# Optimization experiments

Measured on AMD Instinct MI355X. Metric: run time of the kernel, lower is better.

Reference implementation:

```python
import jax, jax.numpy as jnp
import numpy as np

# ---- constants mirroring the module config ----
TIMESTEPS = 1000
N_GT = 3            # GT phases {stable, pre-shock, shock}
NUM_EXPERTS = 6     # 2 sub-experts per GT phase; phase L -> experts {L, L+3}
LAMBDA_REG = 0.01
LAMBDA_LB = 0.01
PHASE_WEIGHTS = np.array([1.0, 5.0, 5.0], dtype=np.float32)


def _sinusoidal_embed(t, dim):
    # standard DDPM sinusoidal timestep embedding -> [B, dim]
    half = dim // 2
    freqs = jnp.exp(-jnp.log(10000.0) * jnp.arange(half, dtype=jnp.float32) / half)
    args = t.astype(jnp.float32)[:, None] * freqs[None, :]
    return jnp.concatenate([jnp.sin(args), jnp.cos(args)], axis=-1)


def _alphas_bar():
    betas = jnp.linspace(1e-4, 0.02, TIMESTEPS, dtype=jnp.float32)
    return jnp.cumprod(1.0 - betas)


def setup_inputs() -> dict:
    B, Tp, Tf, Df, Ds, dm, E, H = 512, 256, 64, 64, 32, 512, NUM_EXPERTS, 512
    key = jax.random.key(0)
    ks = jax.random.split(key, 16)
    s = 0.02  # init scale
    d_in = Df + 2 * dm  # noisy features + global ctx + t embedding
    return {
        'observed_data': jax.random.normal(ks[0], (B, Tp, Df), jnp.float32),
        'future_data':   jax.random.normal(ks[1], (B, Tf, Df), jnp.float32),
        'static_context': jax.random.normal(ks[2], (B, Ds), jnp.float32),
        'eps':           jax.random.normal(ks[3], (B, Tf, Df), jnp.float32),
        'phase_label':   jax.random.randint(ks[4], (B,), 0, N_GT),
        't':             jax.random.randint(ks[5], (B,), 0, TIMESTEPS),
        'W_enc':    jax.random.normal(ks[6], (Df, dm), jnp.float32) * s,
        'b_enc':    jnp.zeros((dm,), jnp.float32),
        'W_stat':   jax.random.normal(ks[7], (Ds, dm), jnp.float32) * s,
        'W_router': jax.random.normal(ks[8], (dm, E), jnp.float32) * s,
        'b_router': jnp.zeros((E,), jnp.float32),
        'W1': jax.random.normal(ks[9],  (E, d_in, H), jnp.float32) * s,
        'b1': jnp.zeros((E, H), jnp.float32),
        'W2': jax.random.normal(ks[10], (E, H, Df), jnp.float32) * s,
        'b2': jnp.zeros((E, Df), jnp.float32),
    }


def reference(observed_data, future_data, static_context, eps,
              W_enc, b_enc, W_stat, W_router, b_router,
              W1, b1, W2, b2, phase_label, t):
    B, Tf, Df = future_data.shape
    E = W1.shape[0]
    dm = W_enc.shape[1]

    # ---- frozen encoder (torch.no_grad in the original) ----
    ctx_seq = jax.nn.gelu(observed_data @ W_enc + (static_context @ W_stat)[:, None, :] + b_enc)  # [B,Tp,dm]
    global_ctx = ctx_seq.mean(axis=1)                                                             # [B,dm]
    ctx_seq = jax.lax.stop_gradient(ctx_seq)
    global_ctx = jax.lax.stop_gradient(global_ctx)

    # ---- router (trainable) ----
    router_logits = global_ctx @ W_router + b_router        # [B,E]
    router_probs = jax.nn.softmax(router_logits, axis=-1)

    # ---- GT-masked top-1 routing: phase p -> argmax over experts {p, p+3} ----
    selected = jnp.zeros((B,), jnp.int32)
    for p in range(N_GT):
        sub = jnp.stack([router_probs[:, p], router_probs[:, p + N_GT]], axis=1)  # [B,2]
        winner = p + N_GT * jnp.argmax(sub, axis=1).astype(jnp.int32)
        selected = jnp.where(phase_label == p, winner, selected)

    # ---- diffusion scheduler: add_noise ----
    ab = _alphas_bar()[t]                                   # [B]
    noisy_fut = (jnp.sqrt(ab)[:, None, None] * future_data
                 + jnp.sqrt(1.0 - ab)[:, None, None] * eps)  # [B,Tf,Df]

    # ---- expert backbones: run all E experts densely, then gather routed output ----
    t_emb = _sinusoidal_embed(t, dm)                        # [B,dm]
    cond = jnp.concatenate([
        noisy_fut,
        jnp.broadcast_to(global_ctx[:, None, :], (B, Tf, dm)),
        jnp.broadcast_to(t_emb[:, None, :],      (B, Tf, dm)),
    ], axis=-1)                                             # [B,Tf,Din]
    h = jax.nn.gelu(jnp.einsum('btd,edh->ebth', cond, W1) + b1[:, None, None, :])
    outputs_all = jnp.einsum('ebth,ehf->ebtf', h, W2) + b2[:, None, None, :]  # [E,B,Tf,Df]

    pred = outputs_all[selected, jnp.arange(B)]             # [B,Tf,Df] gradient-surgery dispatch
    loss_raw = jnp.mean((pred - eps) ** 2, axis=(1, 2))     # per-sample MSE, [B]

    # weighted_loss * count/B summed over experts == mean(loss_raw * w[selected%3])
    lw = jnp.asarray(PHASE_WEIGHTS)
    w_sample = lw[selected % N_GT]
    total_loss = jnp.mean(loss_raw * w_sample)

    # ---- consistency regularization on a fixed 4-sample subset ----
    S = min(B, 4)
    out_sub = outputs_all[:, :S]                            # [E,S,Tf,Df]
    chain = jnp.float32(0.0)
    for i in [0, 1, 3, 4]:
        if i + 1 < E:
            chain += jnp.mean((out_sub[i] - out_sub[i + 1]) ** 2)
    for i in range(N_GT):
        if i + N_GT < E:
            chain += jnp.mean((out_sub[i] - out_sub[i + N_GT]) ** 2)
    diff = out_sub[:, :, 1:] - out_sub[:, :, :-1]
    smooth = jnp.sum(jnp.mean(diff ** 2, axis=(1, 2, 3)))
    total_loss += (chain + 0.5 * smooth) * LAMBDA_REG

    # ---- load-balance loss ----
    onehot = (selected[:, None] == jnp.arange(E)[None, :]).astype(jnp.float32)  # [B,E]
    f = onehot.mean(axis=0)
    P = router_probs.mean(axis=0)
    total_loss += LAMBDA_LB * E * jnp.sum(f * P)

    return total_loss
```

## Files before the change

### kernel.cpp

```cpp
#include <hip/hip_runtime.h>

typedef float  f32x4 __attribute__((ext_vector_type(4)));
typedef short  s16x8 __attribute__((ext_vector_type(8)));
typedef unsigned short u16;
typedef u16    u16x4 __attribute__((ext_vector_type(4)));

#define TIMESTEPS 1000

#define WS_ALPHAS   0
#define WS_FREQS    1024
#define WS_PROBS    1536
#define WS_SELECTED 4608
#define WS_LOSSB    5632
#define WS_META     6144
#define WS_ROWSRC   6400
#define WS_ROWDST   7040
#define WS_PARTS    7680
#define WS_GCTX     8192
#define WS_XC       270336
#define WS_HSTAT    532480
#define WS_HSTAT2   794624
#define WS_OUTSUB   806912
#define WS_U16BYTE  3620864
#define U_WENCT     0
#define U_W1T       32768
#define U_W2T       3375104

__device__ __forceinline__ u16 f2bf(float x){
    unsigned u = __builtin_bit_cast(unsigned, x);
    unsigned r = (u + 0x7FFFu + ((u >> 16) & 1u)) >> 16;
    return (u16)r;
}

__device__ __forceinline__ float gelu_f(float x){
    float x2 = x * x;
    float t  = x * fmaf(0.035677408136f, x2, 0.7978845608028654f);
    float ex = __builtin_amdgcn_exp2f(t * 2.885390081777927f);
    float r  = __builtin_amdgcn_rcpf(ex + 1.0f);
    return fmaf(-x, r, x);
}

__device__ __forceinline__ void mfma16(f32x4& c, s16x8 a, s16x8 b){
    asm volatile("v_mfma_f32_16x16x32_bf16 %0, %1, %2, %0" : "+v"(c) : "v"(a), "v"(b));
}

__global__ __launch_bounds__(256) void k0T(const float* __restrict__ Wenc,
                                           const float* __restrict__ W1,
                                           const float* __restrict__ W2,
                                           u16* __restrict__ uws,
                                           float* __restrict__ ws){
    __shared__ float sT[32][33];
    __shared__ float sp[256];
    int bid = blockIdx.x, tid = threadIdx.x;
    const int t1 = 6*34*16, t2 = t1 + 6*16*2, t3 = t2 + 2*16;
    if(bid == t3){
        for(int k = tid; k < 256; k += 256)
            ws[WS_FREQS + k] = expf(-logf(10000.0f) * (float)k / 256.0f);
        float p = 1.f;
        #pragma unroll
        for(int r = 0; r < 4; r++){
            int i = tid*4 + r;
            if(i < TIMESTEPS){
                float beta = 0.0001f + (0.02f - 0.0001f) * ((float)i / 999.0f);
                p *= (1.0f - beta);
            }
        }
        sp[tid] = p;
        __syncthreads();
        for(int st = 1; st < 256; st <<= 1){
            float v = (tid >= st) ? sp[tid - st] : 1.0f;
            __syncthreads();
            sp[tid] *= v;
            __syncthreads();
        }
        float run = (tid == 0) ? 1.0f : sp[tid - 1];
        for(int r = 0; r < 4; r++){
            int i = tid*4 + r;
            if(i < TIMESTEPS){
                float beta = 0.0001f + (0.02f - 0.0001f) * ((float)i / 999.0f);
                run *= (1.0f - beta);
                ws[WS_ALPHAS + i] = run;
            }
        }
        return;
    }
    const float* src; u16* dst; int K, J, kt, jt;
    if(bid < t1){
        int e = bid / 544, r = bid % 544; kt = r / 16; jt = r % 16;
        src = W1 + (size_t)e*1088*512; dst = uws + U_W1T + (size_t)e*512*1088; K = 1088; J = 512;
    } else if(bid < t2){
        int r = bid - t1; int e = r / 32; r %= 32; kt = r / 2; jt = r % 2;
        src = W2 + (size_t)e*512*64; dst = uws + U_W2T + (size_t)e*64*512; K = 512; J = 64;
    } else {
        int r = bid - t2; kt = r / 16; jt = r % 16;
        src = Wenc; dst = uws + U_WENCT; K = 64; J = 512;
    }
    int ty = tid >> 5, tx = tid & 31;
    #pragma unroll
    for(int i = 0; i < 4; i++)
        sT[ty + i*8][tx] = src[(size_t)(kt*32 + ty + i*8)*J + jt*32 + tx];
    __syncthreads();
    #pragma unroll
    for(int i = 0; i < 4; i++)
        dst[(size_t)(jt*32 + ty + i*8)*K + kt*32 + tx] = f2bf(sT[tx][ty + i*8]);
}

#define PADX 72
__global__ __launch_bounds__(512) void k1_enc_mfma(const float* __restrict__ obs,
        const float* __restrict__ stat, const float* __restrict__ Wstat,
        const float* __restrict__ benc, const u16* __restrict__ uws,
        float* __restrict__ ws){
    __shared__ u16  sX[128 * PADX];
    __shared__ float sBias[512];
    __shared__ float sStat[32];
    int bid = blockIdx.x, b = bid >> 1, q = bid & 1, tid = threadIdx.x;
    if(tid < 32) sStat[tid] = stat[b*32 + tid];
    {
        int row = tid >> 2, c0 = (tid & 3) * 16;
        const f32x4* src = (const f32x4*)&obs[((size_t)(b*256 + q*128 + row))*64 + c0];
        u16* dst = &sX[row*PADX + c0];
        #pragma unroll
        for(int i = 0; i < 4; i++){
            f32x4 v = src[i];
            u16x4 pk; pk.x = f2bf(v.x); pk.y = f2bf(v.y); pk.z = f2bf(v.z); pk.w = f2bf(v.w);
            *(u16x4*)(dst + i*4) = pk;
        }
    }
    __syncthreads();
    {
        float v = benc[tid];
        #pragma unroll 8
        for(int s = 0; s < 32; s++) v += sStat[s] * Wstat[s*512 + tid];
        sBias[tid] = v;
    }
    __syncthreads();
    int w = tid >> 6, l = tid & 63, lr = l & 15, lk = (l >> 4) * 8;
    const u16* wencT = uws + U_WENCT;
    s16x8 bf[4][2];
    float bias[4];
    #pragma unroll
    for(int n = 0; n < 4; n++){
        int col = w*64 + n*16 + lr;
        bf[n][0] = *(const s16x8*)&wencT[col*64 + lk];
        bf[n][1] = *(const s16x8*)&wencT[col*64 + 32 + lk];
        bias[n]  = sBias[col];
    }
    float cac[4] = {0.f, 0.f, 0.f, 0.f};
    for(int mt = 0; mt < 8; mt++){
        s16x8 a0 = *(const s16x8*)&sX[(mt*16 + lr)*PADX + lk];
        s16x8 a1 = *(const s16x8*)&sX[(mt*16 + lr)*PADX + 32 + lk];
        #pragma unroll
        for(int n = 0; n < 4; n++){
            f32x4 acc = {bias[n], bias[n], bias[n], bias[n]};
            mfma16(acc, a0, bf[n][0]);
            mfma16(acc, a1, bf[n][1]);
            cac[n] += gelu_f(acc.x) + gelu_f(acc.y) + gelu_f(acc.z) + gelu_f(acc.w);
        }
    }
    #pragma unroll
    for(int n = 0; n < 4; n++){
        cac[n] += __shfl_xor(cac[n], 16);
        cac[n] += __shfl_xor(cac[n], 32);
    }
    float* pdst = q ? &ws[WS_HSTAT + b*512] : &ws[WS_GCTX + b*512];
    if(l < 16){
        #pragma unroll
        for(int n = 0; n < 4; n++)
            pdst[w*64 + n*16 + l] = cac[n];
    }
}

__global__ __launch_bounds__(64) void k2_router(const float* __restrict__ Wr,
        const float* __restrict__ br, const int* __restrict__ phase,
        const int* __restrict__ t_arr, float* __restrict__ ws){
    int b = blockIdx.x, lane = threadIdx.x;
    float acc[6] = {0,0,0,0,0,0};
    int tv = t_arr[b];
    u16* XC = (u16*)(ws + WS_XC);
    for(int k = 0; k < 8; k++){
        int d = k*64 + lane;
        float gv = (ws[WS_GCTX + b*512 + d] + ws[WS_HSTAT + b*512 + d]) * (1.0f/256.0f);
        XC[b*1024 + d] = f2bf(gv);
        #pragma unroll
        for(int e = 0; e < 6; e++) acc[e] += gv * Wr[d*6 + e];
        float fr = ws[WS_FREQS + (d & 255)];
        float a = (float)tv * fr;
        XC[b*1024 + 512 + d] = f2bf((d < 256) ? sinf(a) : cosf(a));
    }
    #pragma unroll
    for(int off = 32; off > 0; off >>= 1)
        #pragma unroll
        for(int e = 0; e < 6; e++) acc[e] += __shfl_down(acc[e], off);
    if(lane == 0){
        float logit[6], mx = -1e30f;
        #pragma unroll
        for(int e = 0; e < 6; e++){ logit[e] = acc[e] + br[e]; mx = fmaxf(mx, logit[e]); }
        float s = 0.f, p[6];
        #pragma unroll
        for(int e = 0; e < 6; e++){ p[e] = expf(logit[e] - mx); s += p[e]; }
        float inv = 1.0f / s;
        #pragma unroll
        for(int e = 0; e < 6; e++) ws[WS_PROBS + b*6 + e] = p[e] * inv;
        int ph = phase[b];
        int sel = ph + ((logit[ph + 3] > logit[ph]) ? 3 : 0);
        ((int*)ws)[WS_SELECTED + b] = sel;
    }
}

__global__ __launch_bounds__(512) void k2b_group(float* __restrict__ ws){
    __shared__ int sCnt[8][6];
    __shared__ int sBase[8][6];
    __shared__ int sSec[6], sTot[6];
    int tid = threadIdx.x, w = tid >> 6, l = tid & 63;
    int* wsi = (int*)ws;
    int sv = wsi[WS_SELECTED + tid];
    unsigned long long mym = 0;
    #pragma unroll
    for(int e = 0; e < 6; e++){
        unsigned long long m = __ballot(sv == e);
        if(l == 0) sCnt[w][e] = __popcll(m);
        if(sv == e) mym = m;
    }
    __syncthreads();
    if(tid == 0){
        int o = 0;
        for(int e = 0; e < 6; e++){
            sSec[e] = o;
            int t0 = 0;
            for(int ww = 0; ww < 8; ww++){ sBase[ww][e] = o; o += sCnt[ww][e]; t0 += sCnt[ww][e]; }
            sTot[e] = t0;
            o += 4;
        }
        int nch = 0;
        for(int e = 0; e < 6; e++){
            int len = sTot[e] + 4, st = sSec[e];
            for(int s = 0; s < len; s += 64){
                int cl = len - s; if(cl > 64) cl = 64;
                wsi[WS_META + 4 + nch*4 + 0] = e;
                wsi[WS_META + 4 + nch*4 + 1] = st + s;
                wsi[WS_META + 4 + nch*4 + 2] = cl;
                nch++;
            }
        }
        wsi[WS_META] = nch;
    }
    __syncthreads();
    int rank = __popcll(mym & ((1ull << l) - 1ull));
    int pos = sBase[w][sv] + rank;
    wsi[WS_ROWSRC + pos] = tid;
    wsi[WS_ROWDST + pos] = WS_HSTAT + tid*512;
    if(tid < 24){
        int e = tid >> 2, b = tid & 3;
        int pos2 = sSec[e] + sTot[e] + b;
        wsi[WS_ROWSRC + pos2] = b;
        wsi[WS_ROWDST + pos2] = WS_HSTAT2 + (e*4 + b)*512;
    }
}

__global__ __launch_bounds__(256) void k3_hstat(const u16* __restrict__ uws,
        const float* __restrict__ b1, float* __restrict__ ws){
    __shared__ int sSrc[64], sDst[64];
    int bid = blockIdx.x, tid = threadIdx.x;
    int c = bid >> 3, jt = bid & 7;
    int* wsi = (int*)ws;
    if(c >= wsi[WS_META]) return;
    int e    = wsi[WS_META + 4 + c*4 + 0];
    int start= wsi[WS_META + 4 + c*4 + 1];
    int len  = wsi[WS_META + 4 + c*4 + 2];
    if(tid < 64){
        int ok = tid < len;
        sSrc[tid] = ok ? wsi[WS_ROWSRC + start + tid] : 0;
        sDst[tid] = ok ? wsi[WS_ROWDST + start + tid] : -1;
    }
    __syncthreads();
    int w = tid >> 6, l = tid & 63, lr = l & 15, lk = (l >> 4) * 8;
    int col = jt*64 + w*16 + lr;
    const u16* XC = (const u16*)(ws + WS_XC);
    const u16* rowA[4];
    #pragma unroll
    for(int mt = 0; mt < 4; mt++)
        rowA[mt] = XC + (size_t)sSrc[mt*16 + lr]*1024 + lk;
    const u16* bp = uws + U_W1T + ((size_t)e*512 + col)*1088 + 64 + lk;
    f32x4 acc[4];
    {
        float bv = b1[e*512 + col];
        f32x4 z = {bv, bv, bv, bv};
        #pragma unroll
        for(int mt = 0; mt < 4; mt++) acc[mt] = z;
    }
    #pragma unroll 4
    for(int ks = 0; ks < 32; ks++){
        s16x8 bb = *(const s16x8*)(bp + ks*32);
        s16x8 a0 = *(const s16x8*)(rowA[0] + ks*32);
        s16x8 a1 = *(const s16x8*)(rowA[1] + ks*32);
        s16x8 a2 = *(const s16x8*)(rowA[2] + ks*32);
        s16x8 a3 = *(const s16x8*)(rowA[3] + ks*32);
        mfma16(acc[0], a0, bb);
        mfma16(acc[1], a1, bb);
        mfma16(acc[2], a2, bb);
        mfma16(acc[3], a3, bb);
    }
    #pragma unroll
    for(int mt = 0; mt < 4; mt++){
        #pragma unroll
        for(int rg = 0; rg < 4; rg++){
            int r = mt*16 + (l >> 4)*4 + rg;
            int d = sDst[r];
            if(d >= 0) ws[d + col] = acc[mt][rg];
        }
    }
}

#define PADN 72
#define PADH 520
__global__ __launch_bounds__(512) void k4_ffn(const float* __restrict__ fut,
        const float* __restrict__ eps, const int* __restrict__ t_arr,
        const u16* __restrict__ uws, const float* __restrict__ b2,
        float* __restrict__ ws){
    __shared__ u16 sN[64 * PADN];
    __shared__ u16 sH[64 * PADH];
    __shared__ float sHs[512];
    __shared__ float sRed[8];
    int tid = threadIdx.x, bid = blockIdx.x;
    int* wsi = (int*)ws;
    int b, e, store;
    if(bid < 512){ b = bid; e = wsi[WS_SELECTED + b]; store = 0; }
    else { int r = bid - 512; e = r >> 2; b = r & 3; store = 1; }
    sHs[tid] = store ? ws[WS_HSTAT2 + (e*4 + b)*512 + tid] : ws[WS_HSTAT + b*512 + tid];
    int tv = t_arr[b];
    float ab = ws[WS_ALPHAS + tv];
    float sa = sqrtf(ab), sb = sqrtf(1.0f - ab);
    {
        int r = tid >> 3, c0 = (tid & 7) * 8;
        const f32x4* pf = (const f32x4*)&fut[((size_t)b*64 + r)*64 + c0];
        const f32x4* pe = (const f32x4*)&eps[((size_t)b*64 + r)*64 + c0];
        f32x4 f0 = pf[0], f1 = pf[1], e0 = pe[0], e1 = pe[1];
        u16x4 p0, p1;
        p0.x = f2bf(sa*f0.x + sb*e0.x); p0.y = f2bf(sa*f0.y + sb*e0.y);
        p0.z = f2bf(sa*f0.z + sb*e0.z); p0.w = f2bf(sa*f0.w + sb*e0.w);
        p1.x = f2bf(sa*f1.x + sb*e1.x); p1.y = f2bf(sa*f1.y + sb*e1.y);
        p1.z = f2bf(sa*f1.z + sb*e1.z); p1.w = f2bf(sa*f1.w + sb*e1.w);
        *(u16x4*)&sN[r*PADN + c0]     = p0;
        *(u16x4*)&sN[r*PADN + c0 + 4] = p1;
    }
    __syncthreads();
    int w = tid >> 6, l = tid & 63, lr = l & 15, lk = (l >> 4) * 8;
    const u16* w1T = uws + U_W1T;
    const u16* w2T = uws + U_W2T;
    f32x4 hacc[4][4];
    float hb[4];
    s16x8 bw[4][2];
    #pragma unroll
    for(int nt = 0; nt < 4; nt++){
        int col = w*64 + nt*16 + lr;
        hb[nt] = sHs[col];
        bw[nt][0] = *(const s16x8*)&w1T[((size_t)e*512 + col)*1088 + lk];
        bw[nt][1] = *(const s16x8*)&w1T[((size_t)e*512 + col)*1088 + 32 + lk];
    }
    #pragma unroll
    for(int mt = 0; mt < 4; mt++){
        s16x8 a0 = *(const s16x8*)&sN[(mt*16 + lr)*PADN + lk];
        s16x8 a1 = *(const s16x8*)&sN[(mt*16 + lr)*PADN + 32 + lk];
        #pragma unroll
        for(int nt = 0; nt < 4; nt++){
            f32x4 acc = {hb[nt], hb[nt], hb[nt], hb[nt]};
            mfma16(acc, a0, bw[nt][0]);
            mfma16(acc, a1, bw[nt][1]);
            hacc[mt][nt] = acc;
        }
    }
    #pragma unroll
    for(int mt = 0; mt < 4; mt++)
        #pragma unroll
        for(int nt = 0; nt < 4; nt++){
            int col = w*64 + nt*16 + lr;
            #pragma unroll
            for(int rg = 0; rg < 4; rg++){
                int row = mt*16 + (l >> 4)*4 + rg;
                sH[row*PADH + col] = f2bf(gelu_f(hacc[mt][nt][rg]));
            }
        }
    __syncthreads();
    int mtg = (w >> 2) << 1;
    int nt  = w & 3;
    f32x4 oacc[2];
    {
        float bz = b2[e*64 + nt*16 + lr];
        f32x4 z = {bz, bz, bz, bz}; oacc[0] = z; oacc[1] = z;
    }
    for(int ks = 0; ks < 16; ks++){
        s16x8 bb = *(const s16x8*)&w2T[((size_t)e*64 + nt*16 + lr)*512 + ks*32 + lk];
        #pragma unroll
        for(int i = 0; i < 2; i++){
            s16x8 a = *(const s16x8*)&sH[((mtg + i)*16 + lr)*PADH + ks*32 + lk];
            mfma16(oacc[i], a, bb);
        }
    }
    if(store){
        #pragma unroll
        for(int i = 0; i < 2; i++)
            #pragma unroll
            for(int rg = 0; rg < 4; rg++){
                int row = (mtg + i)*16 + (l >> 4)*4 + rg;
                int col = nt*16 + lr;
                ws[WS_OUTSUB + (e*4 + b)*4096 + row*64 + col] = oacc[i][rg];
            }
    } else {
        float ls = 0.f;
        #pragma unroll
        for(int i = 0; i < 2; i++)
            #pragma unroll
            for(int rg = 0; rg < 4; rg++){
                int row = (mtg + i)*16 + (l >> 4)*4 + rg;
                int col = nt*16 + lr;
                float d = oacc[i][rg] - eps[((size_t)b*64 + row)*64 + col];
                ls += d*d;
            }
        #pragma unroll
        for(int off = 32; off > 0; off >>= 1) ls += __shfl_down(ls, off);
        if(l == 0) sRed[w] = ls;
        __syncthreads();
        if(tid == 0){
            float s = 0.f;
            #pragma unroll
            for(int q = 0; q < 8; q++) s += sRed[q];
            const float pw[3] = {1.f, 5.f, 5.f};
            ws[WS_LOSSB + b] = (s * (1.0f/4096.0f)) * pw[e % 3];
        }
    }
}

__global__ __launch_bounds__(256) void k5a_parts(float* __restrict__ ws){
    __shared__ float red[256];
    int bid = blockIdx.x, tid = threadIdx.x;
    float s = 0.f;
    if(bid < 7){
        const int pa[7] = {0,1,3,4,0,1,2};
        const int pb[7] = {1,2,4,5,3,4,5};
        const float* A  = &ws[WS_OUTSUB + pa[bid]*16384];
        const float* Bp = &ws[WS_OUTSUB + pb[bid]*16384];
        for(int i = tid; i < 4096; i += 256){
            f32x4 a = *(const f32x4*)&A[i*4];
            f32x4 c = *(const f32x4*)&Bp[i*4];
            f32x4 d = a - c;
            s += d.x*d.x + d.y*d.y + d.z*d.z + d.w*d.w;
        }
        s *= (1.0f/16384.0f);
    } else {
        int e = bid - 7;
        const float* O = &ws[WS_OUTSUB + e*16384];
        for(int i = tid; i < 4*63*16; i += 256){
            int sm = i / (63*16); int r = i % (63*16);
            int tf = r / 16; int f4 = (r % 16) * 4;
            f32x4 a = *(const f32x4*)&O[(sm*64 + tf + 1)*64 + f4];
            f32x4 c = *(const f32x4*)&O[(sm*64 + tf)*64 + f4];
            f32x4 d = a - c;
            s += d.x*d.x + d.y*d.y + d.z*d.z + d.w*d.w;
        }
        s *= (1.0f/16128.0f) * 0.5f;
    }
    red[tid] = s;
    __syncthreads();
    for(int st = 128; st > 0; st >>= 1){
        if(tid < st) red[tid] += red[tid + st];
        __syncthreads();
    }
    if(tid == 0) ws[WS_PARTS + bid] = red[0];
}

__global__ __launch_bounds__(512) void k5b_final(float* __restrict__ ws, float* __restrict__ out){
    __shared__ float rA[512], rB[512];
    int tid = threadIdx.x;
    int* wsi = (int*)ws;
    int sel = wsi[WS_SELECTED + tid];
    rA[tid] = ws[WS_LOSSB + tid];
    __syncthreads();
    for(int st = 256; st > 0; st >>= 1){ if(tid < st) rA[tid] += rA[tid + st]; __syncthreads(); }
    float total = 0.f;
    if(tid == 0){
        total = rA[0] * (1.0f/512.0f);
        float reg = 0.f;
        for(int p = 0; p < 13; p++) reg += ws[WS_PARTS + p];
        total += 0.01f * reg;
    }
    __syncthreads();
    float lb = 0.f;
    for(int e = 0; e < 6; e++){
        rA[tid] = (sel == e) ? 1.f : 0.f;
        rB[tid] = ws[WS_PROBS + tid*6 + e];
        __syncthreads();
        for(int st = 256; st > 0; st >>= 1){
            if(tid < st){ rA[tid] += rA[tid + st]; rB[tid] += rB[tid + st]; }
            __syncthreads();
        }
        if(tid == 0) lb += (rA[0] * (1.0f/512.f)) * (rB[0] * (1.0f/512.f));
        __syncthreads();
    }
    if(tid == 0) out[0] = total + 0.01f * 6.0f * lb;
}

extern "C" void kernel_launch(void* const* d_in, const int* in_sizes, int n_in,
                              void* d_out, int out_size, void* d_ws, size_t ws_size,
                              hipStream_t stream){
    const float* obs  = (const float*)d_in[0];
    const float* fut  = (const float*)d_in[1];
    const float* stat = (const float*)d_in[2];
    const float* eps  = (const float*)d_in[3];
    const int*   phase= (const int*)d_in[4];
    const int*   t    = (const int*)d_in[5];
    const float* Wenc = (const float*)d_in[6];
    const float* benc = (const float*)d_in[7];
    const float* Wstat= (const float*)d_in[8];
    const float* Wr   = (const float*)d_in[9];
    const float* br   = (const float*)d_in[10];
    const float* W1   = (const float*)d_in[11];
    const float* b1   = (const float*)d_in[12];
    const float* W2   = (const float*)d_in[13];
    const float* b2   = (const float*)d_in[14];
    float* ws  = (float*)d_ws;
    u16*   uws = (u16*)((char*)d_ws + WS_U16BYTE);
    float* out = (float*)d_out;

    k0T<<<3489, 256, 0, stream>>>(Wenc, W1, W2, uws, ws);
    k1_enc_mfma<<<1024, 512, 0, stream>>>(obs, stat, Wstat, benc, uws, ws);
    k2_router<<<512, 64, 0, stream>>>(Wr, br, phase, t, ws);
    k2b_group<<<1, 512, 0, stream>>>(ws);
    k3_hstat<<<112, 256, 0, stream>>>(uws, b1, ws);
    k4_ffn<<<536, 512, 0, stream>>>(fut, eps, t, uws, b2, ws);
    k5a_parts<<<13, 256, 0, stream>>>(ws);
    k5b_final<<<1, 512, 0, stream>>>(ws, out);
}
```

Baseline: 109.5 us.

## Precompute static-context bias in prep kernel, transpose FFN GEMM, shuffle-reduce final

Moves the per-sample static-context projection (stat·Wstat + benc) out of the encoder kernel into extra blocks of the weight-transpose kernel, batching 8 samples per block so each Wstat load is reused. The encoder kernel then only reads a precomputed bias row. The first FFN GEMM is transposed so the W1 tile becomes the A operand, which allows packed 4-wide bf16 stores into sH and removes the large accumulator array. The final reduction kernel replaces repeated shared-memory tree reductions with wavefront shuffles. The cost is extra workspace traffic for the bias buffer.

```diff
diff --git a/kernel.cpp b/kernel.cpp
--- a/kernel.cpp
+++ b/kernel.cpp
@@ -22,6 +22,7 @@
 #define WS_HSTAT2   794624
 #define WS_OUTSUB   806912
 #define WS_U16BYTE  3620864
+#define WS_BIAS     2691072
 #define U_WENCT     0
 #define U_W1T       32768
 #define U_W2T       3375104
@@ -47,13 +48,16 @@
 __global__ __launch_bounds__(256) void k0T(const float* __restrict__ Wenc,
                                            const float* __restrict__ W1,
                                            const float* __restrict__ W2,
+                                           const float* __restrict__ stat,
+                                           const float* __restrict__ Wstat,
+                                           const float* __restrict__ benc,
                                            u16* __restrict__ uws,
                                            float* __restrict__ ws){
     __shared__ float sT[32][33];
-    __shared__ float sp[256];
     int bid = blockIdx.x, tid = threadIdx.x;
     const int t1 = 6*34*16, t2 = t1 + 6*16*2, t3 = t2 + 2*16;
     if(bid == t3){
+        __shared__ float sp[256];
         for(int k = tid; k < 256; k += 256)
             ws[WS_FREQS + k] = expf(-logf(10000.0f) * (float)k / 256.0f);
         float p = 1.f;
@@ -81,6 +85,28 @@
                 run *= (1.0f - beta);
                 ws[WS_ALPHAS + i] = run;
             }
+        }
+        return;
+    }
+    if(bid > t3){
+        __shared__ float sSt[8*32];
+        int g = bid - t3 - 1;
+        int b0 = g*8;
+        sSt[tid & 255] = stat[b0*32 + (tid & 255)];
+        __syncthreads();
+        #pragma unroll
+        for(int half = 0; half < 2; half++){
+            int j = tid + half*256;
+            float acc[8] = {0,0,0,0,0,0,0,0};
+            for(int s = 0; s < 32; s++){
+                float wv = Wstat[s*512 + j];
+                #pragma unroll
+                for(int bb = 0; bb < 8; bb++) acc[bb] += sSt[bb*32 + s] * wv;
+            }
+            float bz = benc[j];
+            #pragma unroll
+            for(int bb = 0; bb < 8; bb++)
+                ws[WS_BIAS + (b0 + bb)*512 + j] = acc[bb] + bz;
         }
         return;
     }
@@ -107,14 +133,10 @@
 
 #define PADX 72
 __global__ __launch_bounds__(512) void k1_enc_mfma(const float* __restrict__ obs,
-        const float* __restrict__ stat, const float* __restrict__ Wstat,
-        const float* __restrict__ benc, const u16* __restrict__ uws,
-        float* __restrict__ ws){
+        const u16* __restrict__ uws, float* __restrict__ ws){
     __shared__ u16  sX[128 * PADX];
     __shared__ float sBias[512];
-    __shared__ float sStat[32];
     int bid = blockIdx.x, b = bid >> 1, q = bid & 1, tid = threadIdx.x;
-    if(tid < 32) sStat[tid] = stat[b*32 + tid];
     {
         int row = tid >> 2, c0 = (tid & 3) * 16;
         const f32x4* src = (const f32x4*)&obs[((size_t)(b*256 + q*128 + row))*64 + c0];
@@ -126,13 +148,7 @@
             *(u16x4*)(dst + i*4) = pk;
         }
     }
-    __syncthreads();
-    {
-        float v = benc[tid];
-        #pragma unroll 8
-        for(int s = 0; s < 32; s++) v += sStat[s] * Wstat[s*512 + tid];
-        sBias[tid] = v;
-    }
+    sBias[tid] = ws[WS_BIAS + b*512 + tid];
     __syncthreads();
     int w = tid >> 6, l = tid & 63, lr = l & 15, lk = (l >> 4) * 8;
     const u16* wencT = uws + U_WENCT;
@@ -347,39 +363,29 @@
     int w = tid >> 6, l = tid & 63, lr = l & 15, lk = (l >> 4) * 8;
     const u16* w1T = uws + U_W1T;
     const u16* w2T = uws + U_W2T;
-    f32x4 hacc[4][4];
-    float hb[4];
-    s16x8 bw[4][2];
+    s16x8 aw[4][2];
+    #pragma unroll
+    for(int mt = 0; mt < 4; mt++){
+        int jrow = w*64 + mt*16 + lr;
+        aw[mt][0] = *(const s16x8*)&w1T[((size_t)e*512 + jrow)*1088 + lk];
+        aw[mt][1] = *(const s16x8*)&w1T[((size_t)e*512 + jrow)*1088 + 32 + lk];
+    }
     #pragma unroll
     for(int nt = 0; nt < 4; nt++){
-        int col = w*64 + nt*16 + lr;
-        hb[nt] = sHs[col];
-        bw[nt][0] = *(const s16x8*)&w1T[((size_t)e*512 + col)*1088 + lk];
-        bw[nt][1] = *(const s16x8*)&w1T[((size_t)e*512 + col)*1088 + 32 + lk];
-    }
-    #pragma unroll
-    for(int mt = 0; mt < 4; mt++){
-        s16x8 a0 = *(const s16x8*)&sN[(mt*16 + lr)*PADN + lk];
-        s16x8 a1 = *(const s16x8*)&sN[(mt*16 + lr)*PADN + 32 + lk];
-        #pragma unroll
-        for(int nt = 0; nt < 4; nt++){
-            f32x4 acc = {hb[nt], hb[nt], hb[nt], hb[nt]};
-            mfma16(acc, a0, bw[nt][0]);
-            mfma16(acc, a1, bw[nt][1]);
-            hacc[mt][nt] = acc;
-        }
-    }
-    #pragma unroll
-    for(int mt = 0; mt < 4; mt++)
-        #pragma unroll
-        for(int nt = 0; nt < 4; nt++){
-            int col = w*64 + nt*16 + lr;
-            #pragma unroll
-            for(int rg = 0; rg < 4; rg++){
-                int row = mt*16 + (l >> 4)*4 + rg;
-                sH[row*PADH + col] = f2bf(gelu_f(hacc[mt][nt][rg]));
-            }
-        }
+        s16x8 nb0 = *(const s16x8*)&sN[(nt*16 + lr)*PADN + lk];
+        s16x8 nb1 = *(const s16x8*)&sN[(nt*16 + lr)*PADN + 32 + lk];
+        #pragma unroll
+        for(int mt = 0; mt < 4; mt++){
+            int j0 = w*64 + mt*16 + (l >> 4)*4;
+            f32x4 acc = *(const f32x4*)&sHs[j0];
+            mfma16(acc, aw[mt][0], nb0);
+            mfma16(acc, aw[mt][1], nb1);
+            u16x4 pk;
+            pk.x = f2bf(gelu_f(acc.x)); pk.y = f2bf(gelu_f(acc.y));
+            pk.z = f2bf(gelu_f(acc.z)); pk.w = f2bf(gelu_f(acc.w));
+            *(u16x4*)&sH[(nt*16 + lr)*PADH + j0] = pk;
+        }
+    }
     __syncthreads();
     int mtg = (w >> 2) << 1;
     int nt  = w & 3;
@@ -469,34 +475,48 @@
 }
 
 __global__ __launch_bounds__(512) void k5b_final(float* __restrict__ ws, float* __restrict__ out){
-    __shared__ float rA[512], rB[512];
-    int tid = threadIdx.x;
+    __shared__ float sW[8];
+    __shared__ float sF[8][6], sP[8][6];
+    int tid = threadIdx.x, w = tid >> 6, l = tid & 63;
     int* wsi = (int*)ws;
     int sel = wsi[WS_SELECTED + tid];
-    rA[tid] = ws[WS_LOSSB + tid];
-    __syncthreads();
-    for(int st = 256; st > 0; st >>= 1){ if(tid < st) rA[tid] += rA[tid + st]; __syncthreads(); }
-    float total = 0.f;
+    float lv = ws[WS_LOSSB + tid];
+    float pv[6], cf[6];
+    #pragma unroll
+    for(int e = 0; e < 6; e++){
+        pv[e] = ws[WS_PROBS + tid*6 + e];
+        cf[e] = (sel == e) ? 1.f : 0.f;
+    }
+    #pragma unroll
+    for(int off = 32; off > 0; off >>= 1){
+        lv += __shfl_down(lv, off);
+        #pragma unroll
+        for(int e = 0; e < 6; e++){
+            pv[e] += __shfl_down(pv[e], off);
+            cf[e] += __shfl_down(cf[e], off);
+        }
+    }
+    if(l == 0){
+        sW[w] = lv;
+        #pragma unroll
+        for(int e = 0; e < 6; e++){ sF[w][e] = cf[e]; sP[w][e] = pv[e]; }
+    }
+    __syncthreads();
     if(tid == 0){
-        total = rA[0] * (1.0f/512.0f);
+        float total = 0.f;
+        for(int q = 0; q < 8; q++) total += sW[q];
+        total *= (1.0f/512.0f);
         float reg = 0.f;
         for(int p = 0; p < 13; p++) reg += ws[WS_PARTS + p];
         total += 0.01f * reg;
-    }
-    __syncthreads();
-    float lb = 0.f;
-    for(int e = 0; e < 6; e++){
-        rA[tid] = (sel == e) ? 1.f : 0.f;
-        rB[tid] = ws[WS_PROBS + tid*6 + e];
-        __syncthreads();
-        for(int st = 256; st > 0; st >>= 1){
-            if(tid < st){ rA[tid] += rA[tid + st]; rB[tid] += rB[tid + st]; }
-            __syncthreads();
-        }
-        if(tid == 0) lb += (rA[0] * (1.0f/512.f)) * (rB[0] * (1.0f/512.f));
-        __syncthreads();
-    }
-    if(tid == 0) out[0] = total + 0.01f * 6.0f * lb;
+        float lb = 0.f;
+        for(int e = 0; e < 6; e++){
+            float f = 0.f, pp = 0.f;
+            for(int q = 0; q < 8; q++){ f += sF[q][e]; pp += sP[q][e]; }
+            lb += (f * (1.0f/512.f)) * (pp * (1.0f/512.f));
+        }
+        out[0] = total + 0.01f * 6.0f * lb;
+    }
 }
 
 extern "C" void kernel_launch(void* const* d_in, const int* in_sizes, int n_in,
@@ -521,8 +541,8 @@
     u16*   uws = (u16*)((char*)d_ws + WS_U16BYTE);
     float* out = (float*)d_out;
 
-    k0T<<<3489, 256, 0, stream>>>(Wenc, W1, W2, uws, ws);
-    k1_enc_mfma<<<1024, 512, 0, stream>>>(obs, stat, Wstat, benc, uws, ws);
+    k0T<<<3553, 256, 0, stream>>>(Wenc, W1, W2, stat, Wstat, benc, uws, ws);
+    k1_enc_mfma<<<1024, 512, 0, stream>>>(obs, uws, ws);
     k2_router<<<512, 64, 0, stream>>>(Wr, br, phase, t, ws);
     k2b_group<<<1, 512, 0, stream>>>(ws);
     k3_hstat<<<112, 256, 0, stream>>>(uws, b1, ws);
```

Measured after the change: 107.8 us. Within noise of the previous version (-1.5%).
